# Kernel optimization log

Hardware: AMD Instinct MI355X
Metric: run time of the kernel (lower is better)

## Reference

```python
import jax, jax.numpy as jnp
import numpy as np

B, N, D = 1, 768, 256
H = 4
HD = D // H
K = 16
EDGE_DIM = 4
LN_EPS = 1e-5


def setup_inputs() -> dict:
    key = jax.random.key(0)
    ks = jax.random.split(key, 16)
    g = lambda k, shape, fan: jax.random.normal(k, shape, jnp.float32) / np.sqrt(fan)
    return {
        'x': jax.random.normal(ks[0], (B, N, D), jnp.float32),
        'Wqkv_w': g(ks[1], (D, 3 * D), D), 'Wqkv_b': jnp.zeros((3 * D,), jnp.float32),
        'out_w': g(ks[2], (D, D), D), 'out_b': jnp.zeros((D,), jnp.float32),
        'ffn1_w': g(ks[3], (2 * D, 2 * D), 2 * D), 'ffn1_b': jnp.zeros((2 * D,), jnp.float32),
        'ln_g': jnp.ones((2 * D,), jnp.float32), 'ln_b': jnp.zeros((2 * D,), jnp.float32),
        'ffn2_w': g(ks[4], (2 * D, D), 2 * D), 'ffn2_b': jnp.zeros((D,), jnp.float32),
        'e1_w': g(ks[5], (EDGE_DIM, 2 * H), EDGE_DIM), 'e1_b': jnp.zeros((2 * H,), jnp.float32),
        'e2_w': g(ks[6], (2 * H, H), 2 * H), 'e2_b': jnp.zeros((H,), jnp.float32),
        'graph_gate': jnp.float32(0.5),
    }


def _normalize(v):
    return v / jnp.clip(jnp.linalg.norm(v, axis=-1, keepdims=True), 1e-12)


def reference(x, Wqkv_w, Wqkv_b, out_w, out_b, ffn1_w, ffn1_b, ln_g, ln_b,
              ffn2_w, ffn2_b, e1_w, e1_b, e2_w, e2_b, graph_gate):
    b, n, d = x.shape
    # ---- graph topology (no grad, discrete top-k) ----
    xs = jax.lax.stop_gradient(x)
    dn_s = _normalize(xs)
    sim_d = jnp.einsum('bnd,bmd->bnm', dn_s, dn_s)
    eye = jnp.eye(n, dtype=bool)
    sim_d = jnp.where(eye, -jnp.inf, sim_d)
    idx = jax.lax.top_k(sim_d, K)[1]                       # (B,N,K)
    adj = jnp.zeros((b, n, n), bool).at[
        jnp.arange(b)[:, None, None], jnp.arange(n)[None, :, None], idx].set(True)
    adj = adj | jnp.swapaxes(adj, 1, 2) | eye              # symmetric + self loops
    # ---- differentiable edge features (B,N,N,4) ----
    dnm = _normalize(x)
    sim = jnp.einsum('bnd,bmd->bnm', dnm, dnm)
    diff = x[:, :, None, :] - x[:, None, :, :]             # (B,N,N,D) memory-bound
    l2 = jnp.linalg.norm(diff, axis=-1) / np.float32(np.sqrt(d))
    ad = jnp.abs(diff)
    ef = jnp.stack([sim, l2, ad.mean(-1), ad.max(-1)], axis=-1)
    # ---- edge bias per head (B,H,N,N) ----
    h = jax.nn.relu(ef @ e1_w + e1_b)
    bias = jnp.transpose(h @ e2_w + e2_b, (0, 3, 1, 2))
    # ---- attention ----
    qkv = (x @ Wqkv_w + Wqkv_b).reshape(b, n, H, HD, 3)
    qkv = jnp.transpose(qkv, (0, 2, 1, 3, 4))              # (B,H,N,HD,3)
    q, k, v = qkv[..., 0], qkv[..., 1], qkv[..., 2]
    logits = jnp.einsum('bhnd,bhmd->bhnm', q, k) / np.float32(np.sqrt(HD))
    logits = logits + graph_gate * bias
    logits = jnp.where(adj[:, None], logits, -jnp.inf)     # sparse masking
    attn = jax.nn.softmax(logits, axis=-1)
    ctx = jnp.einsum('bhnm,bhmd->bhnd', attn, v)
    msg = jnp.transpose(ctx, (0, 2, 1, 3)).reshape(b, n, d) @ out_w + out_b
    # ---- FFN: Linear -> LayerNorm -> GELU -> Linear, residual ----
    y = jnp.concatenate([x, msg], axis=-1) @ ffn1_w + ffn1_b
    mu = y.mean(-1, keepdims=True)
    var = ((y - mu) ** 2).mean(-1, keepdims=True)
    y = (y - mu) / jnp.sqrt(var + LN_EPS) * ln_g + ln_b
    y = jax.nn.gelu(y, approximate=False)
    return x + (y @ ffn2_w + ffn2_b)
```

## Files before the change

kernel.cpp:

```cpp
#include <hip/hip_runtime.h>
#include <hip/hip_bf16.h>
#include <math.h>

#define NN 768
#define DD 256
#define NHEAD 4
#define HDIM 64
#define TOPK 16

typedef __attribute__((ext_vector_type(8))) short short8;
typedef __attribute__((ext_vector_type(4))) float f32x4;

__device__ __forceinline__ unsigned short f2bf(float f) {
    unsigned u = __float_as_uint(f);
    unsigned r = u + 0x7fffu + ((u >> 16) & 1u);
    return (unsigned short)(r >> 16);
}

__global__ __launch_bounds__(256) void k_prep_norms(
        const float* __restrict__ Wqkv,
        const float* __restrict__ outw,
        const float* __restrict__ f1w,  const float* __restrict__ f2w,
        unsigned short* __restrict__ t_qkv,
        unsigned short* __restrict__ t_f1,  unsigned short* __restrict__ t_f2,
        unsigned short* __restrict__ t_g,   unsigned short* __restrict__ t_outn,
        const float* __restrict__ x,
        double* __restrict__ nrm2_d, double* __restrict__ nrm_d,
        double* __restrict__ invn_d,
        unsigned short* __restrict__ xb, unsigned int* __restrict__ adjw) {
    int b = blockIdx.x;
    int tid = threadIdx.x;
    if (b < 576) {
        const float* src; unsigned short* dst; int K, C, tile;
        if (b < 192)      { src = Wqkv; dst = t_qkv; K = 256; C = 768; tile = b; }
        else if (b < 448) { src = f1w;  dst = t_f1;  K = 512; C = 512; tile = b - 192; }
        else              { src = f2w;  dst = t_f2;  K = 512; C = 256; tile = b - 448; }
        int tpr = C / 32;
        int k0 = (tile / tpr) * 32, c0 = (tile % tpr) * 32;
        __shared__ float tls[32][33];
        int r = tid >> 3, c4 = (tid & 7) * 4;
        float4 v = *(const float4*)&src[(size_t)(k0 + r) * C + c0 + c4];
        tls[r][c4 + 0] = v.x; tls[r][c4 + 1] = v.y;
        tls[r][c4 + 2] = v.z; tls[r][c4 + 3] = v.w;
        __syncthreads();
        int rc = tid >> 3, k4 = (tid & 7) * 4;
        unsigned short* d = &dst[(size_t)(c0 + rc) * K + k0 + k4];
        unsigned short w0 = f2bf(tls[k4 + 0][rc]);
        unsigned short w1 = f2bf(tls[k4 + 1][rc]);
        unsigned short w2 = f2bf(tls[k4 + 2][rc]);
        unsigned short w3 = f2bf(tls[k4 + 3][rc]);
        d[0] = w0; d[1] = w1; d[2] = w2; d[3] = w3;
        if (b >= 192 && b < 448 && k0 < 256) {
            unsigned short* d2 = &t_g[(size_t)(c0 + rc) * 512 + k0 + k4];
            d2[0] = w0; d2[1] = w1; d2[2] = w2; d2[3] = w3;
        }
    } else if (b < 768) {
        int nb = b - 576;
        int gid = nb * 256 + tid;
        adjw[gid * 3 + 0] = 0u;
        adjw[gid * 3 + 1] = 0u;
        adjw[gid * 3 + 2] = 0u;
        int n = nb * 4 + (tid >> 6);
        int lane = tid & 63;
        const float* row = x + (size_t)n * DD;
        double s = 0.0;
        #pragma unroll
        for (int i = 0; i < 4; ++i) {
            float v = row[lane + 64 * i];
            xb[(size_t)n * DD + lane + 64 * i] = f2bf(v);
            s += (double)v * (double)v;
        }
        for (int off = 32; off > 0; off >>= 1) s += __shfl_down(s, off);
        if (lane == 0) {
            nrm2_d[n] = s;
            double nv = sqrt(s);
            nrm_d[n] = nv;
            invn_d[n] = 1.0 / fmax(nv, 1e-12);
        }
    } else {
        int idx = (b - 768) * 1024 + tid * 4;
        float4 v = *(const float4*)&outw[idx];
        t_outn[idx + 0] = f2bf(v.x);
        t_outn[idx + 1] = f2bf(v.y);
        t_outn[idx + 2] = f2bf(v.z);
        t_outn[idx + 3] = f2bf(v.w);
    }
}

__global__ __launch_bounds__(512) void k_simqkv(
        const float* __restrict__ x, const double* __restrict__ invn_d,
        double* __restrict__ simd,
        const unsigned short* __restrict__ xbf,
        const unsigned short* __restrict__ t_qkv,
        const float* __restrict__ Wqkv_b,
        float* __restrict__ qb, float* __restrict__ kb, float* __restrict__ vb,
        const unsigned short* __restrict__ t_f1,
        const unsigned short* __restrict__ t_outn,
        unsigned short* __restrict__ t_g,
        const float* __restrict__ out_b, const float* __restrict__ f1w,
        const float* __restrict__ ffn1_b, float* __restrict__ bias_f) {
    __shared__ double Ad[2][32][38];
    __shared__ double Bd[2][32][38];
    int b = blockIdx.x;
    int tid = threadIdx.x;
    if (b < 300) {
        int r = (int)((sqrtf(8.f * (float)b + 1.f) - 1.f) * 0.5f);
        while ((r + 1) * (r + 2) / 2 <= b) ++r;
        while (r * (r + 1) / 2 > b) --r;
        int c = b - r * (r + 1) / 2;
        int n0 = c * 32, m0 = r * 32;

        int g = tid >> 8;
        int t = tid & 255;
        int tx = t & 15, ty = t >> 4;
        int srow = t >> 3;
        int skq  = (t & 7) * 4;
        double d00 = 0.0, d01 = 0.0, d10 = 0.0, d11 = 0.0;

        #pragma unroll
        for (int ch = 0; ch < 4; ++ch) {
            int d0 = g * 128 + ch * 32;
            float4 av = *(const float4*)&x[(size_t)(n0 + srow) * DD + d0 + skq];
            float4 bv = *(const float4*)&x[(size_t)(m0 + srow) * DD + d0 + skq];
            Ad[g][srow][skq + 0] = (double)av.x;
            Ad[g][srow][skq + 1] = (double)av.y;
            Ad[g][srow][skq + 2] = (double)av.z;
            Ad[g][srow][skq + 3] = (double)av.w;
            Bd[g][srow][skq + 0] = (double)bv.x;
            Bd[g][srow][skq + 1] = (double)bv.y;
            Bd[g][srow][skq + 2] = (double)bv.z;
            Bd[g][srow][skq + 3] = (double)bv.w;
            __syncthreads();
            #pragma unroll
            for (int d = 0; d < 32; d += 4) {
                double a0x = Ad[g][ty][d + 0], a0y = Ad[g][ty][d + 1];
                double a0z = Ad[g][ty][d + 2], a0w = Ad[g][ty][d + 3];
                double a1x = Ad[g][ty + 16][d + 0], a1y = Ad[g][ty + 16][d + 1];
                double a1z = Ad[g][ty + 16][d + 2], a1w = Ad[g][ty + 16][d + 3];
                double b0x = Bd[g][tx][d + 0], b0y = Bd[g][tx][d + 1];
                double b0z = Bd[g][tx][d + 2], b0w = Bd[g][tx][d + 3];
                double b1x = Bd[g][tx + 16][d + 0], b1y = Bd[g][tx + 16][d + 1];
                double b1z = Bd[g][tx + 16][d + 2], b1w = Bd[g][tx + 16][d + 3];
                d00 += a0x * b0x + a0y * b0y + a0z * b0z + a0w * b0w;
                d01 += a0x * b1x + a0y * b1y + a0z * b1z + a0w * b1w;
                d10 += a1x * b0x + a1y * b0y + a1z * b0z + a1w * b0w;
                d11 += a1x * b1x + a1y * b1y + a1z * b1z + a1w * b1w;
            }
            __syncthreads();
        }

        double* part = &Ad[0][0][0];
        if (g == 1) {
            part[t * 4 + 0] = d00; part[t * 4 + 1] = d01;
            part[t * 4 + 2] = d10; part[t * 4 + 3] = d11;
        }
        __syncthreads();
        if (g == 0) {
            d00 += part[t * 4 + 0]; d01 += part[t * 4 + 1];
            d10 += part[t * 4 + 2]; d11 += part[t * 4 + 3];
            double in_m0 = invn_d[m0 + tx], in_m1 = invn_d[m0 + tx + 16];
            double in_n0 = invn_d[n0 + ty], in_n1 = invn_d[n0 + ty + 16];
            double v00 = d00 * in_n0 * in_m0;
            double v01 = d01 * in_n0 * in_m1;
            double v10 = d10 * in_n1 * in_m0;
            double v11 = d11 * in_n1 * in_m1;
            simd[(size_t)(n0 + ty) * NN + m0 + tx]           = v00;
            simd[(size_t)(n0 + ty) * NN + m0 + tx + 16]      = v01;
            simd[(size_t)(n0 + ty + 16) * NN + m0 + tx]      = v10;
            simd[(size_t)(n0 + ty + 16) * NN + m0 + tx + 16] = v11;
            simd[(size_t)(m0 + tx) * NN + n0 + ty]           = v00;
            simd[(size_t)(m0 + tx + 16) * NN + n0 + ty]      = v01;
            simd[(size_t)(m0 + tx) * NN + n0 + ty + 16]      = v10;
            simd[(size_t)(m0 + tx + 16) * NN + n0 + ty + 16] = v11;
        }
    } else if (b < 588) {
        int w = tid >> 6, lane = tid & 63;
        int id = (b - 300) * 8 + w;
        int rt = id % 48, ct = id / 48;
        int m0 = rt * 16, n0 = ct * 16;
        int fr = lane & 15, fg = lane >> 4;
        f32x4 acc = {0.f, 0.f, 0.f, 0.f};
        const unsigned short* brow = &t_qkv[(size_t)(n0 + fr) * DD];
        #pragma unroll
        for (int k0 = 0; k0 < DD; k0 += 32) {
            short8 a = *(const short8*)&xbf[(size_t)(m0 + fr) * DD + k0 + fg * 8];
            short8 bb8 = *(const short8*)&brow[k0 + fg * 8];
            acc = __builtin_amdgcn_mfma_f32_16x16x32_bf16(a, bb8, acc, 0, 0, 0);
        }
        int cidx = n0 + fr;
        int hh = cidx / 192, rem = cidx % 192, hd = rem / 3, s = rem % 3;
        float* dst = (s == 0) ? qb : (s == 1) ? kb : vb;
        float bb = Wqkv_b[cidx];
        #pragma unroll
        for (int r = 0; r < 4; ++r) {
            int n = m0 + fg * 4 + r;
            dst[((size_t)hh * NN + n) * HDIM + hd] = acc[r] + bb;
        }
    } else if (b < 652) {
        int w = tid >> 6, lane = tid & 63;
        int id = (b - 588) * 8 + w;
        int m0 = (id & 31) * 16;
        int n0 = (id >> 5) * 16;
        int fr = lane & 15, fg = lane >> 4;
        f32x4 acc = {0.f, 0.f, 0.f, 0.f};
        const unsigned short* arow = &t_f1[(size_t)(m0 + fr) * 512 + 256];
        const unsigned short* brow = &t_outn[(size_t)(n0 + fr) * 256];
        #pragma unroll
        for (int k0 = 0; k0 < 256; k0 += 32) {
            short8 a = *(const short8*)&arow[k0 + fg * 8];
            short8 bb8 = *(const short8*)&brow[k0 + fg * 8];
            acc = __builtin_amdgcn_mfma_f32_16x16x32_bf16(a, bb8, acc, 0, 0, 0);
        }
        #pragma unroll
        for (int r = 0; r < 4; ++r)
            t_g[(size_t)(m0 + fg * 4 + r) * 512 + 256 + n0 + fr] = f2bf(acc[r]);
    } else {
        float s = ffn1_b[tid];
        for (int c = 0; c < 256; ++c)
            s += out_b[c] * f1w[(size_t)(256 + c) * 512 + tid];
        bias_f[tid] = s;
    }
}

__global__ __launch_bounds__(256) void k_topk(const double* __restrict__ simd,
                                              unsigned char* __restrict__ adj) {
    int tid = threadIdx.x;
    int w = tid >> 6, l = tid & 63;
    int n = blockIdx.x * 4 + w;
    const double* row = simd + (size_t)n * NN;
    double v[12];
    #pragma unroll
    for (int i = 0; i < 12; ++i) {
        int m = l + 64 * i;
        v[i] = (m == n) ? -INFINITY : row[m];
    }
    if (l == 0) adj[(size_t)n * NN + n] = 1;

    for (int itr = 0; itr < TOPK; ++itr) {
        double bv = -INFINITY; int bi = 0x7fffffff;
        #pragma unroll
        for (int i = 0; i < 12; ++i) {
            if (v[i] > bv) { bv = v[i]; bi = l + 64 * i; }
        }
        #pragma unroll
        for (int off = 32; off > 0; off >>= 1) {
            double ov = __shfl_down(bv, off);
            int    oi = __shfl_down(bi, off);
            if (ov > bv || (ov == bv && oi < bi)) { bv = ov; bi = oi; }
        }
        bi = __shfl(bi, 0);
        if ((bi & 63) == l) {
            int slot = bi >> 6;
            #pragma unroll
            for (int i = 0; i < 12; ++i) if (i == slot) v[i] = -INFINITY;
        }
        if (l == 0) {
            adj[(size_t)n * NN + bi] = 1;
            adj[(size_t)bi * NN + n] = 1;
        }
    }
}

__global__ __launch_bounds__(256) void k_edge_attn(
        const float* __restrict__ x,
        const double* __restrict__ nrm2_d,
        const double* __restrict__ nrm_d,
        const double* __restrict__ simd,
        const unsigned char* __restrict__ adj,
        const float* __restrict__ e1_w, const float* __restrict__ e1_b,
        const float* __restrict__ e2_w, const float* __restrict__ e2_b,
        const float* __restrict__ gate_p,
        const float* __restrict__ q, const float* __restrict__ k,
        const float* __restrict__ v,
        unsigned short* __restrict__ ctxb) {
    int n = blockIdx.x;
    int tid = threadIdx.x;
    int w = tid >> 6, l = tid & 63;
    __shared__ unsigned short idxs[NN];
    __shared__ float w_sh[NHEAD][NN];
    __shared__ float ef2s[NN];
    __shared__ float ef3s[NN];
    __shared__ float qsh[NHEAD][HDIM];
    __shared__ int wtot[4];

    int c = 0; int loc[3];
    #pragma unroll
    for (int i = 0; i < 3; ++i) {
        int m = 3 * tid + i;
        if (adj[(size_t)n * NN + m]) loc[c++] = m;
    }
    int pc = c;
    #pragma unroll
    for (int off = 1; off < 64; off <<= 1) {
        int o = __shfl_up(pc, off);
        if (l >= off) pc += o;
    }
    if (l == 63) wtot[w] = pc;
    qsh[w][l] = q[((size_t)w * NN + n) * HDIM + l];
    __syncthreads();
    int base = 0;
    #pragma unroll
    for (int ww = 0; ww < 4; ++ww) if (ww < w) base += wtot[ww];
    int start = base + pc - c;
    for (int i = 0; i < c; ++i) idxs[start + i] = (unsigned short)loc[i];
    int cnt = wtot[0] + wtot[1] + wtot[2] + wtot[3];
    __syncthreads();

    float xa[4];
    #pragma unroll
    for (int i = 0; i < 4; ++i) xa[i] = x[(size_t)n * DD + l + 64 * i];

    for (int j = w; j < cnt; j += 4) {
        int m = idxs[j];
        float sab = 0.f, mab = 0.f;
        #pragma unroll
        for (int i = 0; i < 4; ++i) {
            float xb = x[(size_t)m * DD + l + 64 * i];
            float ad = fabsf(xa[i] - xb);
            sab += ad;
            mab = fmaxf(mab, ad);
        }
        #pragma unroll
        for (int off = 32; off > 0; off >>= 1) {
            sab += __shfl_xor(sab, off);
            mab = fmaxf(mab, __shfl_xor(mab, off));
        }
        if (l == 0) { ef2s[j] = sab * (1.f / 256.f); ef3s[j] = mab; }
    }
    __syncthreads();

    double nrm2n = nrm2_d[n];
    double nrmn  = nrm_d[n];
    float gate = gate_p[0];
    for (int j0 = 0; j0 < cnt; j0 += 64) {
        int j = j0 + (tid >> 2);
        int hh = tid & 3;
        if (j < cnt) {
            int m = idxs[j];
            double s_d   = simd[(size_t)n * NN + m];
            double nrm2m = nrm2_d[m];
            double dotd  = s_d * nrmn * nrm_d[m];
            double l2sq  = fmax(nrm2n + nrm2m - 2.0 * dotd, 0.0);
            float ef0 = (float)s_d;
            float ef1 = (float)(sqrt(l2sq) * (1.0 / 16.0));
            float ef2 = ef2s[j];
            float ef3 = ef3s[j];
            float bb = e2_b[hh];
            #pragma unroll
            for (int jj = 0; jj < 8; ++jj) {
                float hv = e1_b[jj] + ef0 * e1_w[0 * 8 + jj] + ef1 * e1_w[1 * 8 + jj]
                         + ef2 * e1_w[2 * 8 + jj] + ef3 * e1_w[3 * 8 + jj];
                bb += fmaxf(hv, 0.f) * e2_w[jj * 4 + hh];
            }
            w_sh[hh][j] = gate * bb;
        }
    }
    __syncthreads();

    int h = w;
    float lmax = -INFINITY;
    for (int j = l; j < cnt; j += 64) {
        int m = idxs[j];
        const float4* kr = (const float4*)(k + ((size_t)h * NN + m) * HDIM);
        float dotv = 0.f;
        #pragma unroll
        for (int d4 = 0; d4 < HDIM / 4; ++d4) {
            float4 kv = kr[d4];
            dotv += qsh[h][4 * d4 + 0] * kv.x + qsh[h][4 * d4 + 1] * kv.y
                  + qsh[h][4 * d4 + 2] * kv.z + qsh[h][4 * d4 + 3] * kv.w;
        }
        w_sh[h][j] = dotv * 0.125f + w_sh[h][j];
        lmax = fmaxf(lmax, w_sh[h][j]);
    }
    #pragma unroll
    for (int off = 32; off > 0; off >>= 1)
        lmax = fmaxf(lmax, __shfl_xor(lmax, off));

    float lsum = 0.f;
    for (int j = l; j < cnt; j += 64) {
        float e = expf(w_sh[h][j] - lmax);
        w_sh[h][j] = e;
        lsum += e;
    }
    #pragma unroll
    for (int off = 32; off > 0; off >>= 1) lsum += __shfl_xor(lsum, off);
    float inv = 1.f / lsum;
    __syncthreads();

    float acc = 0.f;
    #pragma unroll 4
    for (int j = 0; j < cnt; ++j)
        acc += w_sh[h][j] * v[((size_t)h * NN + idxs[j]) * HDIM + l];
    ctxb[(size_t)n * DD + h * HDIM + l] = f2bf(acc * inv);
}

template<int KD, int MODE, bool CONCAT>
__global__ __launch_bounds__(256) void k_gemm_reg(const unsigned short* __restrict__ A,
                                                  const unsigned short* __restrict__ A2,
                                                  const unsigned short* __restrict__ Bt,
                                                  const float* __restrict__ bias,
                                                  const float* __restrict__ resid,
                                                  float* __restrict__ out,
                                                  unsigned short* __restrict__ outb,
                                                  int ncols) {
    int tid = threadIdx.x;
    int w = tid >> 6, lane = tid & 63;
    int m0 = blockIdx.y * 64 + w * 16;
    int n0 = blockIdx.x * 16;
    int fr = lane & 15, fg = lane >> 4;
    f32x4 acc = {0.f, 0.f, 0.f, 0.f};

    const unsigned short* brow = &Bt[(size_t)(n0 + fr) * KD];
    #pragma unroll
    for (int k0 = 0; k0 < KD; k0 += 32) {
        const unsigned short* Asrc = A; int koff = k0;
        if (CONCAT && k0 >= 256) { Asrc = A2; koff = k0 - 256; }
        int lda = CONCAT ? 256 : KD;
        short8 a = *(const short8*)&Asrc[(size_t)(m0 + fr) * lda + koff + fg * 8];
        short8 b = *(const short8*)&brow[k0 + fg * 8];
        acc = __builtin_amdgcn_mfma_f32_16x16x32_bf16(a, b, acc, 0, 0, 0);
    }

    int cidx = n0 + fr;
    float bb = bias[cidx];
    #pragma unroll
    for (int r = 0; r < 4; ++r) {
        int n = m0 + fg * 4 + r;
        float val = acc[r] + bb;
        if (MODE == 1) val += resid[(size_t)n * ncols + cidx];
        if (MODE == 3) outb[(size_t)n * ncols + cidx] = f2bf(val);
        else           out [(size_t)n * ncols + cidx] = val;
    }
}

__global__ __launch_bounds__(256) void k_ln_gelu(const float* __restrict__ y,
                                                 const float* __restrict__ g,
                                                 const float* __restrict__ b,
                                                 unsigned short* __restrict__ ybb) {
    int n = blockIdx.x;
    int tid = threadIdx.x;
    const float* row = y + (size_t)n * 512;
    __shared__ float red[256];
    float v0 = row[tid], v1 = row[tid + 256];

    red[tid] = v0 + v1; __syncthreads();
    for (int s = 128; s > 0; s >>= 1) {
        if (tid < s) red[tid] += red[tid + s];
        __syncthreads();
    }
    float mu = red[0] * (1.f / 512.f);
    __syncthreads();

    float d0 = v0 - mu, d1 = v1 - mu;
    red[tid] = d0 * d0 + d1 * d1; __syncthreads();
    for (int s = 128; s > 0; s >>= 1) {
        if (tid < s) red[tid] += red[tid + s];
        __syncthreads();
    }
    float var = red[0] * (1.f / 512.f);
    float rstd = 1.f / sqrtf(var + 1e-5f);

    float z0 = d0 * rstd * g[tid] + b[tid];
    float z1 = d1 * rstd * g[tid + 256] + b[tid + 256];
    float o0 = 0.5f * z0 * (1.f + erff(z0 * 0.70710678118654752f));
    float o1 = 0.5f * z1 * (1.f + erff(z1 * 0.70710678118654752f));
    ybb[(size_t)n * 512 + tid]       = f2bf(o0);
    ybb[(size_t)n * 512 + tid + 256] = f2bf(o1);
}

extern "C" void kernel_launch(void* const* d_in, const int* in_sizes, int n_in,
                              void* d_out, int out_size, void* d_ws, size_t ws_size,
                              hipStream_t stream) {
    const float* x       = (const float*)d_in[0];
    const float* Wqkv_w  = (const float*)d_in[1];
    const float* Wqkv_b  = (const float*)d_in[2];
    const float* out_w   = (const float*)d_in[3];
    const float* out_b   = (const float*)d_in[4];
    const float* ffn1_w  = (const float*)d_in[5];
    const float* ffn1_b  = (const float*)d_in[6];
    const float* ln_g    = (const float*)d_in[7];
    const float* ln_b    = (const float*)d_in[8];
    const float* ffn2_w  = (const float*)d_in[9];
    const float* ffn2_b  = (const float*)d_in[10];
    const float* e1_w    = (const float*)d_in[11];
    const float* e1_b    = (const float*)d_in[12];
    const float* e2_w    = (const float*)d_in[13];
    const float* e2_b    = (const float*)d_in[14];
    const float* gate    = (const float*)d_in[15];

    char* base = (char*)d_ws;
    double* simd   = (double*)base;            base += (size_t)NN * NN * 8;
    double* nrm2_d = (double*)base;            base += NN * 8;
    double* nrm_d  = (double*)base;            base += NN * 8;
    double* invn_d = (double*)base;            base += NN * 8;
    float* qb      = (float*)base;             base += (size_t)NN * DD * 4;
    float* kb      = (float*)base;             base += (size_t)NN * DD * 4;
    float* vb      = (float*)base;             base += (size_t)NN * DD * 4;
    float* yb      = (float*)base;             base += (size_t)NN * 512 * 4;
    unsigned char* adj = (unsigned char*)base;  base += (size_t)NN * NN;
    unsigned short* xbf  = (unsigned short*)base; base += (size_t)NN * DD * 2;
    unsigned short* ctxb = (unsigned short*)base; base += (size_t)NN * DD * 2;
    unsigned short* ybb  = (unsigned short*)base; base += (size_t)NN * 512 * 2;
    unsigned short* t_qkv = (unsigned short*)base; base += (size_t)768 * 256 * 2;
    unsigned short* t_f1  = (unsigned short*)base; base += (size_t)512 * 512 * 2;
    unsigned short* t_f2  = (unsigned short*)base; base += (size_t)256 * 512 * 2;
    unsigned short* t_g   = (unsigned short*)base; base += (size_t)512 * 512 * 2;
    unsigned short* t_outn = (unsigned short*)base; base += (size_t)256 * 256 * 2;
    float* bias_f  = (float*)base;             base += 512 * 4;

    k_prep_norms<<<832, 256, 0, stream>>>(Wqkv_w, out_w, ffn1_w, ffn2_w,
                                          t_qkv, t_f1, t_f2, t_g, t_outn,
                                          x, nrm2_d, nrm_d, invn_d, xbf,
                                          (unsigned int*)adj);

    k_simqkv<<<653, 512, 0, stream>>>(x, invn_d, simd, xbf, t_qkv, Wqkv_b,
                                      qb, kb, vb, t_f1, t_outn, t_g,
                                      out_b, ffn1_w, ffn1_b, bias_f);

    k_topk<<<192, 256, 0, stream>>>(simd, adj);

    k_edge_attn<<<NN, 256, 0, stream>>>(x, nrm2_d, nrm_d, simd, adj,
                                        e1_w, e1_b, e2_w, e2_b, gate,
                                        qb, kb, vb, ctxb);

    k_gemm_reg<512, 0, true><<<dim3(32, 12), 256, 0, stream>>>(
        xbf, ctxb, t_g, bias_f, nullptr, yb, nullptr, 512);

    k_ln_gelu<<<NN, 256, 0, stream>>>(yb, ln_g, ln_b, ybb);

    k_gemm_reg<512, 1, false><<<dim3(16, 12), 256, 0, stream>>>(
        ybb, nullptr, t_f2, ffn2_b, x, (float*)d_out, nullptr, DD);
}
```

Before: 72.30 us.

## Compute fp64 similarity matrix with MFMA f64 instead of scalar tiles

```diff
diff --git a/kernel.cpp b/kernel.cpp
--- a/kernel.cpp
+++ b/kernel.cpp
@@ -10,6 +10,7 @@
 
 typedef __attribute__((ext_vector_type(8))) short short8;
 typedef __attribute__((ext_vector_type(4))) float f32x4;
+typedef __attribute__((ext_vector_type(4))) double f64x4;
 
 __device__ __forceinline__ unsigned short f2bf(float f) {
     unsigned u = __float_as_uint(f);
@@ -27,7 +28,8 @@
         const float* __restrict__ x,
         double* __restrict__ nrm2_d, double* __restrict__ nrm_d,
         double* __restrict__ invn_d,
-        unsigned short* __restrict__ xb, unsigned int* __restrict__ adjw) {
+        unsigned short* __restrict__ xb, double* __restrict__ xd,
+        unsigned int* __restrict__ adjw, float* __restrict__ flag) {
     int b = blockIdx.x;
     int tid = threadIdx.x;
     if (b < 576) {
@@ -68,6 +70,7 @@
         for (int i = 0; i < 4; ++i) {
             float v = row[lane + 64 * i];
             xb[(size_t)n * DD + lane + 64 * i] = f2bf(v);
+            xd[(size_t)n * DD + lane + 64 * i] = (double)v;
             s += (double)v * (double)v;
         }
         for (int off = 32; off > 0; off >>= 1) s += __shfl_down(s, off);
@@ -77,18 +80,36 @@
             nrm_d[n] = nv;
             invn_d[n] = 1.0 / fmax(nv, 1e-12);
         }
-    } else {
+    } else if (b < 832) {
         int idx = (b - 768) * 1024 + tid * 4;
         float4 v = *(const float4*)&outw[idx];
         t_outn[idx + 0] = f2bf(v.x);
         t_outn[idx + 1] = f2bf(v.y);
         t_outn[idx + 2] = f2bf(v.z);
         t_outn[idx + 3] = f2bf(v.w);
+    } else {
+        if (tid < 64) {
+            int fr = tid & 15, fg = tid >> 4;
+            double a  = (double)(fr + 2 * fg);
+            double bv = (double)(3 * fg - fr);
+            f64x4 z = {0.0, 0.0, 0.0, 0.0};
+            f64x4 d = __builtin_amdgcn_mfma_f64_16x16x4f64(a, bv, z, 0, 0, 0);
+            bool ok = true;
+            #pragma unroll
+            for (int r = 0; r < 4; ++r) {
+                double i = (double)(fg * 4 + r), j = (double)fr;
+                double exp = 18.0 * i - 4.0 * i * j + 84.0 - 12.0 * j;
+                ok = ok && (d[r] == exp);
+            }
+            unsigned long long good = __ballot(ok ? 1 : 0);
+            if (tid == 0) flag[0] = (good == 0xFFFFFFFFFFFFFFFFull) ? 1.f : 0.f;
+        }
     }
 }
 
 __global__ __launch_bounds__(512) void k_simqkv(
-        const float* __restrict__ x, const double* __restrict__ invn_d,
+        const float* __restrict__ x,
+        const double* __restrict__ xd, const double* __restrict__ invn_d,
         double* __restrict__ simd,
         const unsigned short* __restrict__ xbf,
         const unsigned short* __restrict__ t_qkv,
@@ -98,12 +119,16 @@
         const unsigned short* __restrict__ t_outn,
         unsigned short* __restrict__ t_g,
         const float* __restrict__ out_b, const float* __restrict__ f1w,
-        const float* __restrict__ ffn1_b, float* __restrict__ bias_f) {
+        const float* __restrict__ ffn1_b, float* __restrict__ bias_f,
+        const float* __restrict__ flag) {
     __shared__ double Ad[2][32][38];
     __shared__ double Bd[2][32][38];
     int b = blockIdx.x;
     int tid = threadIdx.x;
+    int w = tid >> 6, lane = tid & 63;
+    int fr = lane & 15, fg = lane >> 4;
     if (b < 300) {
+        if (flag[0] != 0.f) return;
         int r = (int)((sqrtf(8.f * (float)b + 1.f) - 1.f) * 0.5f);
         while ((r + 1) * (r + 2) / 2 <= b) ++r;
         while (r * (r + 1) / 2 > b) --r;
@@ -174,11 +199,9 @@
             simd[(size_t)(m0 + tx + 16) * NN + n0 + ty + 16] = v11;
         }
     } else if (b < 588) {
-        int w = tid >> 6, lane = tid & 63;
         int id = (b - 300) * 8 + w;
         int rt = id % 48, ct = id / 48;
         int m0 = rt * 16, n0 = ct * 16;
-        int fr = lane & 15, fg = lane >> 4;
         f32x4 acc = {0.f, 0.f, 0.f, 0.f};
         const unsigned short* brow = &t_qkv[(size_t)(n0 + fr) * DD];
         #pragma unroll
@@ -197,11 +220,9 @@
             dst[((size_t)hh * NN + n) * HDIM + hd] = acc[r] + bb;
         }
     } else if (b < 652) {
-        int w = tid >> 6, lane = tid & 63;
         int id = (b - 588) * 8 + w;
         int m0 = (id & 31) * 16;
         int n0 = (id >> 5) * 16;
-        int fr = lane & 15, fg = lane >> 4;
         f32x4 acc = {0.f, 0.f, 0.f, 0.f};
         const unsigned short* arow = &t_f1[(size_t)(m0 + fr) * 512 + 256];
         const unsigned short* brow = &t_outn[(size_t)(n0 + fr) * 256];
@@ -214,11 +235,31 @@
         #pragma unroll
         for (int r = 0; r < 4; ++r)
             t_g[(size_t)(m0 + fg * 4 + r) * 512 + 256 + n0 + fr] = f2bf(acc[r]);
-    } else {
+    } else if (b == 652) {
         float s = ffn1_b[tid];
         for (int c = 0; c < 256; ++c)
             s += out_b[c] * f1w[(size_t)(256 + c) * 512 + tid];
         bias_f[tid] = s;
+    } else {
+        if (flag[0] == 0.f) return;
+        int id = (b - 653) * 8 + w;
+        int n0 = (id % 48) * 16, m0 = (id / 48) * 16;
+        f64x4 acc = {0.0, 0.0, 0.0, 0.0};
+        const double* arow = &xd[(size_t)(n0 + fr) * DD];
+        const double* brow = &xd[(size_t)(m0 + fr) * DD];
+        #pragma unroll 8
+        for (int k0 = 0; k0 < DD; k0 += 4) {
+            double a = arow[k0 + fg];
+            double bv = brow[k0 + fg];
+            acc = __builtin_amdgcn_mfma_f64_16x16x4f64(a, bv, acc, 0, 0, 0);
+        }
+        int col = m0 + fr;
+        double in_c = invn_d[col];
+        #pragma unroll
+        for (int r = 0; r < 4; ++r) {
+            int row = n0 + fg * 4 + r;
+            simd[(size_t)row * NN + col] = acc[r] * invn_d[row] * in_c;
+        }
     }
 }
 
@@ -490,6 +531,7 @@
 
     char* base = (char*)d_ws;
     double* simd   = (double*)base;            base += (size_t)NN * NN * 8;
+    double* xd     = (double*)base;            base += (size_t)NN * DD * 8;
     double* nrm2_d = (double*)base;            base += NN * 8;
     double* nrm_d  = (double*)base;            base += NN * 8;
     double* invn_d = (double*)base;            base += NN * 8;
@@ -507,15 +549,16 @@
     unsigned short* t_g   = (unsigned short*)base; base += (size_t)512 * 512 * 2;
     unsigned short* t_outn = (unsigned short*)base; base += (size_t)256 * 256 * 2;
     float* bias_f  = (float*)base;             base += 512 * 4;
-
-    k_prep_norms<<<832, 256, 0, stream>>>(Wqkv_w, out_w, ffn1_w, ffn2_w,
+    float* flag    = (float*)base;             base += 16;
+
+    k_prep_norms<<<833, 256, 0, stream>>>(Wqkv_w, out_w, ffn1_w, ffn2_w,
                                           t_qkv, t_f1, t_f2, t_g, t_outn,
-                                          x, nrm2_d, nrm_d, invn_d, xbf,
-                                          (unsigned int*)adj);
-
-    k_simqkv<<<653, 512, 0, stream>>>(x, invn_d, simd, xbf, t_qkv, Wqkv_b,
+                                          x, nrm2_d, nrm_d, invn_d, xbf, xd,
+                                          (unsigned int*)adj, flag);
+
+    k_simqkv<<<941, 512, 0, stream>>>(x, xd, invn_d, simd, xbf, t_qkv, Wqkv_b,
                                       qb, kb, vb, t_f1, t_outn, t_g,
-                                      out_b, ffn1_w, ffn1_b, bias_f);
+                                      out_b, ffn1_w, ffn1_b, bias_f, flag);
 
     k_topk<<<192, 256, 0, stream>>>(simd, adj);
 
```

After: 72.69 us. No clear change (+0.5%).
